# Optimization experiments

Measured on AMD Instinct MI355X. Metric: run time of the kernel, lower is better.

Reference implementation:

```python
import jax, jax.numpy as jnp
import numpy as np

NOUT1, NOUT2, NBINS, NFEAT = 12, 15, 4000, 6

def setup_inputs() -> dict:
    key = jax.random.key(0)
    ks = jax.random.split(key, 7)
    x = jax.random.normal(ks[0], (64, NFEAT, 500), dtype=jnp.float32)
    # Linear params stored torch-style: W[out, in], b[out]
    W1 = jax.random.normal(ks[1], (NOUT1, NFEAT), dtype=jnp.float32) * (1.0 / np.sqrt(NFEAT))
    b1 = jax.random.normal(ks[2], (NOUT1,), dtype=jnp.float32) * 0.01
    W2 = jax.random.normal(ks[3], (NOUT2, NOUT1), dtype=jnp.float32) * (1.0 / np.sqrt(NOUT1))
    b2 = jax.random.normal(ks[4], (NOUT2,), dtype=jnp.float32) * 0.01
    W3 = jax.random.normal(ks[5], (NBINS, NOUT2), dtype=jnp.float32) * (1.0 / np.sqrt(NOUT2))
    b3 = jax.random.normal(ks[6], (NBINS,), dtype=jnp.float32) * 0.01
    return {"x": x, "W1": W1, "b1": b1, "W2": W2, "b2": b2, "W3": W3, "b3": b3}

def _leaky(h):
    return jnp.where(h >= 0, h, 0.01 * h)

def reference(x, W1, b1, W2, b2, W3, b3):
    nEvts = x.shape[0]
    t = x.reshape(nEvts, NFEAT, -1).transpose(0, 2, 1)      # (E, T, 6)
    h = _leaky(jnp.einsum('etf,of->eto', t, W1) + b1)        # (E, T, 12)
    h = _leaky(jnp.einsum('eti,oi->eto', h, W2) + b2)        # (E, T, 15)
    h = jnp.einsum('eti,oi->eto', h, W3) + b3                # (E, T, 4000)
    h = jax.nn.softplus(h)
    return jnp.sum(h, axis=1)                                # (E, 4000)
```

## Files before the change

kernel.cpp:

```cpp
#include <hip/hip_runtime.h>

#define NOUT1 12
#define NOUT2 15
#define NBINS 4000
#define NFEAT 6
#define NT    500
#define NTPAD 512
#define NEVT  64
#define LOG2E 1.4426950408889634f
#define LN2   0.6931471805599453f

typedef __attribute__((ext_vector_type(8))) short bf16x8;
typedef __attribute__((ext_vector_type(4))) float f32x4;
typedef __attribute__((ext_vector_type(2))) float f32x2;

__device__ __forceinline__ float leaky(float s) {
    return s >= 0.0f ? s : 0.01f * s;
}

__device__ __forceinline__ unsigned short f32_to_bf16_rne(float x) {
    unsigned int u = __float_as_uint(x);
    unsigned int r = (u + 0x7fffu + ((u >> 16) & 1u)) >> 16;
    return (unsigned short)r;
}
__device__ __forceinline__ float bf16_to_f32(unsigned short h) {
    return __uint_as_float((unsigned int)h << 16);
}

__device__ __forceinline__ void sp2_acc(f32x2 d, f32x2& acc) {
    f32x2 u;
    u.x = __builtin_amdgcn_exp2f(-__builtin_fabsf(d.x));
    u.y = __builtin_amdgcn_exp2f(-__builtin_fabsf(d.y));
    acc += __builtin_elementwise_max(d, (f32x2)0.0f);
    f32x2 q = __builtin_elementwise_fma(u, (f32x2)0.175167f, (f32x2)(-0.602758f));
    q = __builtin_elementwise_fma(u, q, (f32x2)1.428718f);
    acc = __builtin_elementwise_fma(u, q, acc);
}

__device__ __forceinline__ void h2_row(
    const float* __restrict__ x, int e, int t,
    const float* __restrict__ W1, const float* __restrict__ b1,
    const float* __restrict__ W2, const float* __restrict__ b2,
    unsigned int packed[16])
{
    float f[NFEAT];
    #pragma unroll
    for (int i = 0; i < NFEAT; ++i)
        f[i] = x[e * NFEAT * NT + i * NT + t];

    float h1[NOUT1];
    #pragma unroll
    for (int o = 0; o < NOUT1; ++o) {
        float s = b1[o];
        #pragma unroll
        for (int i = 0; i < NFEAT; ++i)
            s = fmaf(f[i], W1[o * NFEAT + i], s);
        h1[o] = leaky(s);
    }

    unsigned short hi[16], lo[16];
    #pragma unroll
    for (int o = 0; o < NOUT2; ++o) {
        float s = b2[o];
        #pragma unroll
        for (int i = 0; i < NOUT1; ++i)
            s = fmaf(h1[i], W2[o * NOUT1 + i], s);
        float h2 = leaky(s);
        unsigned short hh = f32_to_bf16_rne(h2);
        hi[o] = hh;
        lo[o] = f32_to_bf16_rne(h2 - bf16_to_f32(hh));
    }
    hi[15] = 0; lo[15] = 0;
    #pragma unroll
    for (int j = 0; j < 8; ++j) {
        packed[j]     = (unsigned int)hi[2*j] | ((unsigned int)hi[2*j+1] << 16);
        packed[8 + j] = (unsigned int)lo[2*j] | ((unsigned int)lo[2*j+1] << 16);
    }
}

__global__ __launch_bounds__(256) void h2_prep(
    const float* __restrict__ x,
    const float* __restrict__ W1, const float* __restrict__ b1,
    const float* __restrict__ W2, const float* __restrict__ b2,
    uint4* __restrict__ ws)
{
    const int e = blockIdx.x;
    const int t = blockIdx.y * 256 + threadIdx.x;
    unsigned int packed[16];
    if (t < NT) {
        h2_row(x, e, t, W1, b1, W2, b2, packed);
    } else {
        #pragma unroll
        for (int j = 0; j < 16; ++j) packed[j] = 0;
    }
    uint4* dst = ws + (size_t)e * 2048 + (t >> 4) * 64 + (t & 15);
    #pragma unroll
    for (int g = 0; g < 4; ++g)
        dst[g * 16] = make_uint4(packed[4*g+0], packed[4*g+1], packed[4*g+2], packed[4*g+3]);
}

__device__ __forceinline__ void kde_phase2(
    const uint4* __restrict__ h2lds,
    const float* __restrict__ W3, const float* __restrict__ b3,
    float* __restrict__ out, int chunk, int e, int tid)
{
    const int wid  = tid >> 6;
    const int lane = tid & 63;
    const int col  = lane & 15;
    const int kg   = lane >> 4;
    const int binbase = chunk * 128 + wid * 16;
    if (binbase >= NBINS) return;
    const int  bin = binbase + col;
    const bool vb  = (bin < NBINS);

    bf16x8 B1, B2;
    const bool hi_first = (kg < 2);
    #pragma unroll
    for (int j = 0; j < 8; ++j) {
        const int kk = (kg * 8 + j) & 15;
        float w = (vb && kk < NOUT2) ? W3[bin * NOUT2 + kk] * LOG2E : 0.0f;
        unsigned short h = f32_to_bf16_rne(w);
        unsigned short l = f32_to_bf16_rne(w - bf16_to_f32(h));
        B1[j] = (short)(hi_first ? h : l);
        B2[j] = (short)(hi_first ? l : h);
    }

    const float bias = vb ? b3[bin] * LOG2E : 0.0f;
    f32x4 bias4 = {bias, bias, bias, bias};

    f32x2 acc01 = {0.0f, 0.0f}, acc23 = {0.0f, 0.0f};
    const bf16x8* ap = reinterpret_cast<const bf16x8*>(h2lds + kg * 16 + col);

    #define TILE_BODY(areg)                                                        \
        {                                                                          \
            f32x4 acc = __builtin_amdgcn_mfma_f32_16x16x32_bf16(areg, B1, bias4, 0, 0, 0); \
            acc = __builtin_amdgcn_mfma_f32_16x16x32_bf16(areg, B2, acc, 0, 0, 0); \
            f32x2 p01 = {acc[0], acc[1]};                                          \
            f32x2 p23 = {acc[2], acc[3]};                                          \
            sp2_acc(p01, acc01);                                                   \
            sp2_acc(p23, acc23);                                                   \
        }

    bf16x8 A[4];
    A[0] = ap[0 * 64];
    A[1] = ap[1 * 64];
    A[2] = ap[2 * 64];
    A[3] = ap[3 * 64];

    #pragma unroll
    for (int g = 0; g < 31; ++g) {
        bf16x8 cur = A[g & 3];
        if (g + 4 < 32)
            A[g & 3] = ap[(g + 4) * 64];
        TILE_BODY(cur)
    }
    {
        bf16x8 cur = A[31 & 3];
        f32x4 acc = __builtin_amdgcn_mfma_f32_16x16x32_bf16(cur, B1, bias4, 0, 0, 0);
        acc = __builtin_amdgcn_mfma_f32_16x16x32_bf16(cur, B2, acc, 0, 0, 0);
        if (kg == 0) {
            f32x2 p01 = {acc[0], acc[1]};
            f32x2 p23 = {acc[2], acc[3]};
            sp2_acc(p01, acc01);
            sp2_acc(p23, acc23);
        }
    }
    #undef TILE_BODY

    float sum = acc01.x + acc01.y + acc23.x + acc23.y;
    sum += __shfl_xor(sum, 16);
    sum += __shfl_xor(sum, 32);
    if (lane < 16 && vb)
        out[e * NBINS + bin] = sum * LN2;
}

__global__ __launch_bounds__(512, 8) void kde_main(
    const uint4* __restrict__ ws,
    const float* __restrict__ W3, const float* __restrict__ b3,
    float* __restrict__ out)
{
    __shared__ uint4 h2lds[2048];
    const int tid   = threadIdx.x;
    const int chunk = blockIdx.x;
    const int e     = blockIdx.y;

    #pragma unroll
    for (int k = 0; k < 4; ++k)
        h2lds[tid + k * 512] = ws[(size_t)e * 2048 + tid + k * 512];
    __syncthreads();

    kde_phase2(h2lds, W3, b3, out, chunk, e, tid);
}

__global__ __launch_bounds__(512, 2) void kde_fused(
    const float* __restrict__ x,
    const float* __restrict__ W1, const float* __restrict__ b1,
    const float* __restrict__ W2, const float* __restrict__ b2,
    const float* __restrict__ W3, const float* __restrict__ b3,
    float* __restrict__ out)
{
    __shared__ uint4 h2lds[2048];
    const int tid   = threadIdx.x;
    const int chunk = blockIdx.x;
    const int e     = blockIdx.y;

    {
        unsigned int packed[16];
        if (tid < NT) {
            h2_row(x, e, tid, W1, b1, W2, b2, packed);
        } else {
            #pragma unroll
            for (int j = 0; j < 16; ++j) packed[j] = 0;
        }
        uint4* dst = &h2lds[(tid >> 4) * 64 + (tid & 15)];
        #pragma unroll
        for (int g = 0; g < 4; ++g)
            dst[g * 16] = make_uint4(packed[4*g+0], packed[4*g+1], packed[4*g+2], packed[4*g+3]);
    }
    __syncthreads();

    kde_phase2(h2lds, W3, b3, out, chunk, e, tid);
}

extern "C" void kernel_launch(void* const* d_in, const int* in_sizes, int n_in,
                              void* d_out, int out_size, void* d_ws, size_t ws_size,
                              hipStream_t stream) {
    const float* x  = (const float*)d_in[0];
    const float* W1 = (const float*)d_in[1];
    const float* b1 = (const float*)d_in[2];
    const float* W2 = (const float*)d_in[3];
    const float* b2 = (const float*)d_in[4];
    const float* W3 = (const float*)d_in[5];
    const float* b3 = (const float*)d_in[6];
    float* out = (float*)d_out;

    const size_t ws_needed = (size_t)NEVT * 2048 * sizeof(uint4);
    if (ws_size >= ws_needed) {
        dim3 pgrid(NEVT, 2);
        h2_prep<<<pgrid, 256, 0, stream>>>(x, W1, b1, W2, b2, (uint4*)d_ws);
        dim3 grid(32, NEVT);
        kde_main<<<grid, 512, 0, stream>>>((const uint4*)d_ws, W3, b3, out);
    } else {
        dim3 grid(32, NEVT);
        kde_fused<<<grid, 512, 0, stream>>>(x, W1, b1, W2, b2, W3, b3, out);
    }
}
```

Baseline: 45.12 us.

## Switch KDE matmul from split-bf16 to single fp16 MFMA with folded bias

Replaces the hi/lo bf16 split (two 16x16x32 MFMAs per tile) with a single fp16 16x16x16 MFMA per tile. The bias is folded in as a 16th K element: h2 carries a constant 1 and W3 carries b3. A new w3_prep kernel pre-converts W3 and b3 to packed fp16 once, so the main kernel no longer converts them per block. This halves MFMA count and LDS/workspace footprint but lowers precision to single fp16, which risks accuracy for large activations.

```diff
diff --git a/kernel.cpp b/kernel.cpp
--- a/kernel.cpp
+++ b/kernel.cpp
@@ -10,21 +10,12 @@
 #define LOG2E 1.4426950408889634f
 #define LN2   0.6931471805599453f
 
-typedef __attribute__((ext_vector_type(8))) short bf16x8;
+typedef __attribute__((ext_vector_type(4))) _Float16 f16x4;
 typedef __attribute__((ext_vector_type(4))) float f32x4;
 typedef __attribute__((ext_vector_type(2))) float f32x2;
 
 __device__ __forceinline__ float leaky(float s) {
     return s >= 0.0f ? s : 0.01f * s;
-}
-
-__device__ __forceinline__ unsigned short f32_to_bf16_rne(float x) {
-    unsigned int u = __float_as_uint(x);
-    unsigned int r = (u + 0x7fffu + ((u >> 16) & 1u)) >> 16;
-    return (unsigned short)r;
-}
-__device__ __forceinline__ float bf16_to_f32(unsigned short h) {
-    return __uint_as_float((unsigned int)h << 16);
 }
 
 __device__ __forceinline__ void sp2_acc(f32x2 d, f32x2& acc) {
@@ -37,11 +28,15 @@
     acc = __builtin_elementwise_fma(u, q, acc);
 }
 
-__device__ __forceinline__ void h2_row(
+__device__ __forceinline__ unsigned short f16bits(float v) {
+    return __builtin_bit_cast(unsigned short, (_Float16)v);
+}
+
+__device__ __forceinline__ void h2_row_f16(
     const float* __restrict__ x, int e, int t,
     const float* __restrict__ W1, const float* __restrict__ b1,
     const float* __restrict__ W2, const float* __restrict__ b2,
-    unsigned int packed[16])
+    unsigned int packed[8])
 {
     float f[NFEAT];
     #pragma unroll
@@ -58,90 +53,84 @@
         h1[o] = leaky(s);
     }
 
-    unsigned short hi[16], lo[16];
+    unsigned short hf[16];
     #pragma unroll
     for (int o = 0; o < NOUT2; ++o) {
         float s = b2[o];
         #pragma unroll
         for (int i = 0; i < NOUT1; ++i)
             s = fmaf(h1[i], W2[o * NOUT1 + i], s);
-        float h2 = leaky(s);
-        unsigned short hh = f32_to_bf16_rne(h2);
-        hi[o] = hh;
-        lo[o] = f32_to_bf16_rne(h2 - bf16_to_f32(hh));
-    }
-    hi[15] = 0; lo[15] = 0;
-    #pragma unroll
-    for (int j = 0; j < 8; ++j) {
-        packed[j]     = (unsigned int)hi[2*j] | ((unsigned int)hi[2*j+1] << 16);
-        packed[8 + j] = (unsigned int)lo[2*j] | ((unsigned int)lo[2*j+1] << 16);
-    }
+        hf[o] = f16bits(leaky(s));
+    }
+    hf[15] = f16bits(1.0f);
+    #pragma unroll
+    for (int j = 0; j < 8; ++j)
+        packed[j] = (unsigned int)hf[2*j] | ((unsigned int)hf[2*j+1] << 16);
 }
 
 __global__ __launch_bounds__(256) void h2_prep(
     const float* __restrict__ x,
     const float* __restrict__ W1, const float* __restrict__ b1,
     const float* __restrict__ W2, const float* __restrict__ b2,
-    uint4* __restrict__ ws)
+    uint2* __restrict__ wsA)
 {
     const int e = blockIdx.x;
     const int t = blockIdx.y * 256 + threadIdx.x;
-    unsigned int packed[16];
+    unsigned int packed[8];
     if (t < NT) {
-        h2_row(x, e, t, W1, b1, W2, b2, packed);
+        h2_row_f16(x, e, t, W1, b1, W2, b2, packed);
     } else {
         #pragma unroll
-        for (int j = 0; j < 16; ++j) packed[j] = 0;
-    }
-    uint4* dst = ws + (size_t)e * 2048 + (t >> 4) * 64 + (t & 15);
+        for (int j = 0; j < 8; ++j) packed[j] = 0;
+    }
+    uint2* dst = wsA + (size_t)e * 2048 + (t >> 4) * 64 + (t & 15);
+    dst[0]  = make_uint2(packed[0], packed[1]);
+    dst[16] = make_uint2(packed[2], packed[3]);
+    dst[32] = make_uint2(packed[4], packed[5]);
+    dst[48] = make_uint2(packed[6], packed[7]);
+}
+
+__global__ __launch_bounds__(256) void w3_prep(
+    const float* __restrict__ W3, const float* __restrict__ b3,
+    uint2* __restrict__ wsB)
+{
+    const int bin = blockIdx.x * 256 + threadIdx.x;
+    if (bin >= NBINS) return;
+    unsigned short wf[16];
+    #pragma unroll
+    for (int k = 0; k < NOUT2; ++k)
+        wf[k] = f16bits(W3[bin * NOUT2 + k] * LOG2E);
+    wf[15] = f16bits(b3[bin] * LOG2E);
+    uint2* dst = wsB + (size_t)bin * 4;
     #pragma unroll
     for (int g = 0; g < 4; ++g)
-        dst[g * 16] = make_uint4(packed[4*g+0], packed[4*g+1], packed[4*g+2], packed[4*g+3]);
+        dst[g] = make_uint2((unsigned int)wf[4*g] | ((unsigned int)wf[4*g+1] << 16),
+                            (unsigned int)wf[4*g+2] | ((unsigned int)wf[4*g+3] << 16));
 }
 
 __device__ __forceinline__ void kde_phase2(
-    const uint4* __restrict__ h2lds,
-    const float* __restrict__ W3, const float* __restrict__ b3,
-    float* __restrict__ out, int chunk, int e, int tid)
-{
-    const int wid  = tid >> 6;
-    const int lane = tid & 63;
-    const int col  = lane & 15;
-    const int kg   = lane >> 4;
-    const int binbase = chunk * 128 + wid * 16;
-    if (binbase >= NBINS) return;
-    const int  bin = binbase + col;
-    const bool vb  = (bin < NBINS);
-
-    bf16x8 B1, B2;
-    const bool hi_first = (kg < 2);
-    #pragma unroll
-    for (int j = 0; j < 8; ++j) {
-        const int kk = (kg * 8 + j) & 15;
-        float w = (vb && kk < NOUT2) ? W3[bin * NOUT2 + kk] * LOG2E : 0.0f;
-        unsigned short h = f32_to_bf16_rne(w);
-        unsigned short l = f32_to_bf16_rne(w - bf16_to_f32(h));
-        B1[j] = (short)(hi_first ? h : l);
-        B2[j] = (short)(hi_first ? l : h);
-    }
-
-    const float bias = vb ? b3[bin] * LOG2E : 0.0f;
-    f32x4 bias4 = {bias, bias, bias, bias};
-
+    const uint2* __restrict__ h2lds,
+    f16x4 B1, float* __restrict__ out, int binbase, int e, int lane)
+{
+    const int col = lane & 15;
+    const int kg  = lane >> 4;
+    const int bin = binbase + col;
+
+    const f32x4 zero4 = {0.0f, 0.0f, 0.0f, 0.0f};
     f32x2 acc01 = {0.0f, 0.0f}, acc23 = {0.0f, 0.0f};
-    const bf16x8* ap = reinterpret_cast<const bf16x8*>(h2lds + kg * 16 + col);
+    const uint2* ap = h2lds + kg * 16 + col;
 
     #define TILE_BODY(areg)                                                        \
         {                                                                          \
-            f32x4 acc = __builtin_amdgcn_mfma_f32_16x16x32_bf16(areg, B1, bias4, 0, 0, 0); \
-            acc = __builtin_amdgcn_mfma_f32_16x16x32_bf16(areg, B2, acc, 0, 0, 0); \
-            f32x2 p01 = {acc[0], acc[1]};                                          \
-            f32x2 p23 = {acc[2], acc[3]};                                          \
+            f16x4 av = __builtin_bit_cast(f16x4, areg);                            \
+            f32x4 c = __builtin_amdgcn_mfma_f32_16x16x16f16(av, B1, zero4, 0, 0, 0); \
+            f32x2 p01 = {c[0], c[1]};                                              \
+            f32x2 p23 = {c[2], c[3]};                                              \
             sp2_acc(p01, acc01);                                                   \
             sp2_acc(p23, acc23);                                                   \
         }
 
-    bf16x8 A[4];
+    uint2 A[4];
     A[0] = ap[0 * 64];
     A[1] = ap[1 * 64];
     A[2] = ap[2 * 64];
@@ -149,47 +138,59 @@
 
     #pragma unroll
     for (int g = 0; g < 31; ++g) {
-        bf16x8 cur = A[g & 3];
+        uint2 cur = A[g & 3];
         if (g + 4 < 32)
             A[g & 3] = ap[(g + 4) * 64];
         TILE_BODY(cur)
     }
     {
-        bf16x8 cur = A[31 & 3];
-        f32x4 acc = __builtin_amdgcn_mfma_f32_16x16x32_bf16(cur, B1, bias4, 0, 0, 0);
-        acc = __builtin_amdgcn_mfma_f32_16x16x32_bf16(cur, B2, acc, 0, 0, 0);
+        f16x4 av = __builtin_bit_cast(f16x4, A[3]);
+        f32x4 c = __builtin_amdgcn_mfma_f32_16x16x16f16(av, B1, zero4, 0, 0, 0);
         if (kg == 0) {
-            f32x2 p01 = {acc[0], acc[1]};
-            f32x2 p23 = {acc[2], acc[3]};
+            f32x2 p01 = {c[0], c[1]};
+            f32x2 p23 = {c[2], c[3]};
             sp2_acc(p01, acc01);
             sp2_acc(p23, acc23);
         }
     }
     #undef TILE_BODY
 
-    float sum = acc01.x + acc01.y + acc23.x + acc23.y;
+    f32x2 s2 = acc01 + acc23;
+    float sum = s2.x + s2.y;
     sum += __shfl_xor(sum, 16);
     sum += __shfl_xor(sum, 32);
-    if (lane < 16 && vb)
+    if (lane < 16 && bin < NBINS)
         out[e * NBINS + bin] = sum * LN2;
 }
 
 __global__ __launch_bounds__(512, 8) void kde_main(
-    const uint4* __restrict__ ws,
-    const float* __restrict__ W3, const float* __restrict__ b3,
+    const uint2* __restrict__ wsA, const uint2* __restrict__ wsB,
     float* __restrict__ out)
 {
-    __shared__ uint4 h2lds[2048];
+    __shared__ uint2 h2lds[2048];
     const int tid   = threadIdx.x;
     const int chunk = blockIdx.x;
     const int e     = blockIdx.y;
 
-    #pragma unroll
-    for (int k = 0; k < 4; ++k)
-        h2lds[tid + k * 512] = ws[(size_t)e * 2048 + tid + k * 512];
+    {
+        uint4* l4 = reinterpret_cast<uint4*>(h2lds);
+        const uint4* g4 = reinterpret_cast<const uint4*>(wsA + (size_t)e * 2048);
+        l4[tid]       = g4[tid];
+        l4[tid + 512] = g4[tid + 512];
+    }
+
+    const int wid  = tid >> 6;
+    const int lane = tid & 63;
+    const int binbase = chunk * 128 + wid * 16;
+    const int col = lane & 15;
+    const int kg  = lane >> 4;
+    const int binc = (binbase + col < NBINS) ? binbase + col : NBINS - 1;
+    f16x4 B1 = __builtin_bit_cast(f16x4, wsB[(size_t)binc * 4 + kg]);
+
     __syncthreads();
-
-    kde_phase2(h2lds, W3, b3, out, chunk, e, tid);
+    if (binbase >= NBINS) return;
+
+    kde_phase2(h2lds, B1, out, binbase, e, lane);
 }
 
 __global__ __launch_bounds__(512, 2) void kde_fused(
@@ -199,27 +200,45 @@
     const float* __restrict__ W3, const float* __restrict__ b3,
     float* __restrict__ out)
 {
-    __shared__ uint4 h2lds[2048];
+    __shared__ uint2 h2lds[2048];
     const int tid   = threadIdx.x;
     const int chunk = blockIdx.x;
     const int e     = blockIdx.y;
 
     {
-        unsigned int packed[16];
+        unsigned int packed[8];
         if (tid < NT) {
-            h2_row(x, e, tid, W1, b1, W2, b2, packed);
+            h2_row_f16(x, e, tid, W1, b1, W2, b2, packed);
         } else {
             #pragma unroll
-            for (int j = 0; j < 16; ++j) packed[j] = 0;
+            for (int j = 0; j < 8; ++j) packed[j] = 0;
         }
-        uint4* dst = &h2lds[(tid >> 4) * 64 + (tid & 15)];
-        #pragma unroll
-        for (int g = 0; g < 4; ++g)
-            dst[g * 16] = make_uint4(packed[4*g+0], packed[4*g+1], packed[4*g+2], packed[4*g+3]);
-    }
+        uint2* dst = &h2lds[(tid >> 4) * 64 + (tid & 15)];
+        dst[0]  = make_uint2(packed[0], packed[1]);
+        dst[16] = make_uint2(packed[2], packed[3]);
+        dst[32] = make_uint2(packed[4], packed[5]);
+        dst[48] = make_uint2(packed[6], packed[7]);
+    }
+
+    const int wid  = tid >> 6;
+    const int lane = tid & 63;
+    const int binbase = chunk * 128 + wid * 16;
+    const int col = lane & 15;
+    const int kg  = lane >> 4;
+    const int binc = (binbase + col < NBINS) ? binbase + col : NBINS - 1;
+    f16x4 B1;
+    #pragma unroll
+    for (int j = 0; j < 4; ++j) {
+        const int kk = kg * 4 + j;
+        float w = (kk < NOUT2) ? W3[binc * NOUT2 + kk] * LOG2E
+                               : b3[binc] * LOG2E;
+        B1[j] = (_Float16)w;
+    }
+
     __syncthreads();
-
-    kde_phase2(h2lds, W3, b3, out, chunk, e, tid);
+    if (binbase >= NBINS) return;
+
+    kde_phase2(h2lds, B1, out, binbase, e, lane);
 }
 
 extern "C" void kernel_launch(void* const* d_in, const int* in_sizes, int n_in,
@@ -234,12 +253,16 @@
     const float* b3 = (const float*)d_in[6];
     float* out = (float*)d_out;
 
-    const size_t ws_needed = (size_t)NEVT * 2048 * sizeof(uint4);
-    if (ws_size >= ws_needed) {
+    const size_t wsA_bytes = (size_t)NEVT * 2048 * sizeof(uint2);
+    const size_t wsB_bytes = (size_t)NBINS * 4 * sizeof(uint2);
+    if (ws_size >= wsA_bytes + wsB_bytes) {
+        uint2* wsA = (uint2*)d_ws;
+        uint2* wsB = (uint2*)((char*)d_ws + wsA_bytes);
         dim3 pgrid(NEVT, 2);
-        h2_prep<<<pgrid, 256, 0, stream>>>(x, W1, b1, W2, b2, (uint4*)d_ws);
+        h2_prep<<<pgrid, 256, 0, stream>>>(x, W1, b1, W2, b2, wsA);
+        w3_prep<<<16, 256, 0, stream>>>(W3, b3, wsB);
         dim3 grid(32, NEVT);
-        kde_main<<<grid, 512, 0, stream>>>((const uint4*)d_ws, W3, b3, out);
+        kde_main<<<grid, 512, 0, stream>>>(wsA, wsB, out);
     } else {
         dim3 grid(32, NEVT);
         kde_fused<<<grid, 512, 0, stream>>>(x, W1, b1, W2, b2, W3, b3, out);
```

After: 37.92 us. -16.0%, faster.
